# Performance work log

Measured on AMD Instinct MI355X. Metric: run time of the kernel, lower is better.

## Reference

```python
import jax, jax.numpy as jnp
import numpy as np

NH, NOPE_D, ROPE_D, V_D, R = 16, 48, 16, 64, 128
EPS = 1e-6

def rms_norm(x, w):
    norm = jax.lax.rsqrt(jnp.mean(jnp.square(x), axis=-1, keepdims=True) + EPS)
    return x * norm * w

def apply_rope(x, cos, sin):
    # x: (..., rope_d); cos/sin broadcastable (..., rope_d//2)
    d = x.shape[-1]
    x1, x2 = x[..., : d // 2], x[..., d // 2 :]
    return jnp.concatenate([x1 * cos - x2 * sin, x2 * cos + x1 * sin], axis=-1)

def setup_inputs() -> dict:
    key = jax.random.key(0)
    ks = jax.random.split(key, 8)
    B, T, D = 2, 2048, 1024
    s = lambda fan_in: 1.0 / np.sqrt(fan_in)
    return {
        "x": jax.random.normal(ks[0], (B, T, D), jnp.float32),
        "cos": jax.random.uniform(ks[1], (T, ROPE_D // 2), jnp.float32),
        "sin": jax.random.uniform(ks[2], (T, ROPE_D // 2), jnp.float32),
        "Wq": jax.random.normal(ks[3], (NH * (NOPE_D + ROPE_D), D), jnp.float32) * s(D),
        "q_norm_w": jnp.ones((NOPE_D + ROPE_D,), jnp.float32),
        "Wkva": jax.random.normal(ks[4], (R + ROPE_D, D), jnp.float32) * s(D),
        "kva_norm_w": jnp.ones((R,), jnp.float32),
        "Wkvb": jax.random.normal(ks[5], (NH * (NOPE_D + V_D), R), jnp.float32) * s(R),
        "Wo": jax.random.normal(ks[6], (D, NH * V_D), jnp.float32) * s(NH * V_D),
    }

def reference(x, cos, sin, Wq, q_norm_w, Wkva, kva_norm_w, Wkvb, Wo):
    B, T, D = x.shape
    # Q path: project, per-head RMSNorm over (nope+rope) dims, split
    q = (x @ Wq.T).reshape(B, T, NH, NOPE_D + ROPE_D)
    q = rms_norm(q, q_norm_w)
    q_nope, q_rope = q[..., :NOPE_D], q[..., NOPE_D:]
    # Low-rank KV path
    kv_a = x @ Wkva.T  # (B,T,R+ROPE_D)
    kv_latent = rms_norm(kv_a[..., :R], kva_norm_w)
    k_rope_raw = kv_a[..., R:]  # (B,T,ROPE_D) shared across heads
    kv_b = (kv_latent @ Wkvb.T).reshape(B, T, NH, NOPE_D + V_D)
    k_nope, v = kv_b[..., :NOPE_D], kv_b[..., NOPE_D:]
    # Decoupled RoPE
    cos_t = cos[None, :T, None, :]  # (1,T,1,rope_d/2)
    sin_t = sin[None, :T, None, :]
    q_rope = apply_rope(q_rope, cos_t, sin_t)
    k_rope = apply_rope(k_rope_raw[:, :, None, :], cos[None, :T, None, :], sin[None, :T, None, :])
    k_rope = jnp.broadcast_to(k_rope, (B, T, NH, ROPE_D))
    q_full = jnp.concatenate([q_nope, q_rope], axis=-1)  # (B,T,NH,64)
    k_full = jnp.concatenate([k_nope, k_rope], axis=-1)
    # Causal attention, scale = 1/sqrt(nope+rope)
    scale = (NOPE_D + ROPE_D) ** -0.5
    scores = jnp.einsum("bqhd,bkhd->bhqk", q_full, k_full) * scale
    causal = jnp.tril(jnp.ones((T, T), bool))
    scores = jnp.where(causal[None, None], scores, -jnp.inf)
    attn = jax.nn.softmax(scores, axis=-1)
    out = jnp.einsum("bhqk,bkhd->bqhd", attn, v).reshape(B, T, NH * V_D)
    return out @ Wo.T
```

## Files before the change

kernel.cpp:

```cpp
#include <hip/hip_runtime.h>
#include <hip/hip_bf16.h>
#include <math.h>

#define NH 16
#define T_ 2048
#define B_ 2
#define D_ 1024
#define EPS 1e-6f

typedef __attribute__((ext_vector_type(8))) short bf16x8;
typedef __attribute__((ext_vector_type(4))) float f32x4;

__device__ __forceinline__ float wred_sum(float v){
  #pragma unroll
  for (int o = 32; o > 0; o >>= 1) v += __shfl_xor(v, o, 64);
  return v;
}

__device__ __forceinline__ unsigned pack_bf16(float a, float b){
  __hip_bfloat162 t = __float22bfloat162_rn(make_float2(a, b));
  unsigned r; __builtin_memcpy(&r, &t, 4); return r;
}

__device__ __forceinline__ void gload_lds16(const void* g, void* l){
  __builtin_amdgcn_global_load_lds((const __attribute__((address_space(1))) void*)g,
                                   (__attribute__((address_space(3))) void*)l, 16, 0, 0);
}

__global__ __launch_bounds__(256)
void cvt5(const float* __restrict__ x, const float* __restrict__ wq,
          const float* __restrict__ wkva, const float* __restrict__ wkvb,
          const float* __restrict__ wo,
          __hip_bfloat16* __restrict__ xb, __hip_bfloat16* __restrict__ wqb,
          __hip_bfloat16* __restrict__ wkvab, __hip_bfloat16* __restrict__ wkvbb,
          __hip_bfloat16* __restrict__ wob)
{
  const int i = blockIdx.x * 256 + threadIdx.x;
  const float* s; __hip_bfloat16* d; size_t soff, doff;
  if      (i < 1048576) { s = x;    d = xb;    soff = doff = i; }
  else if (i < 1310720) { s = wq;   d = wqb;   soff = doff = i - 1048576; }
  else if (i < 1347584) { s = wkva; d = wkvab; soff = doff = i - 1310720; }
  else if (i < 1404928) {
    const int off = i - 1347584;
    const int srow = off >> 5, c4 = off & 31;
    const int h = srow / 112, dd = srow % 112;
    const int drow = (dd < 48) ? (h*48 + dd) : (768 + h*64 + (dd - 48));
    s = wkvb; d = wkvbb; soff = off; doff = (size_t)drow*32 + c4;
  }
  else                  { s = wo;   d = wob;   soff = doff = i - 1404928; }
  float4 v = *(const float4*)(s + soff * 4);
  *(__hip_bfloat162*)(d + doff * 4)     = __float22bfloat162_rn(make_float2(v.x, v.y));
  *(__hip_bfloat162*)(d + doff * 4 + 2) = __float22bfloat162_rn(make_float2(v.z, v.w));
}

template<typename CT>
__global__ __launch_bounds__(256, 2)
void gemm_bt64(const __hip_bfloat16* __restrict__ A, const __hip_bfloat16* __restrict__ W,
               CT* __restrict__ C, int M, int N, int K)
{
  __shared__ __hip_bfloat16 As[2][128 * 64];
  __shared__ __hip_bfloat16 Ws[2][64 * 64];
  const int tid = threadIdx.x;
  const int wv = tid >> 6, lane = tid & 63;
  const int m = lane & 15, quad = lane >> 4;
  const int bm = blockIdx.y * 128, bn = blockIdx.x * 64;

  const __hip_bfloat16* ga[4];
  const __hip_bfloat16* gw[2];
  #pragma unroll
  for (int i = 0; i < 4; i++) {
    const int slot = i*256 + tid;
    const int row = slot >> 3, cb = slot & 7;
    ga[i] = A + (size_t)(bm + row) * K + ((cb ^ (row & 7)) << 3);
  }
  #pragma unroll
  for (int i = 0; i < 2; i++) {
    const int slot = i*256 + tid;
    const int row = slot >> 3, cb = slot & 7;
    int wr = bn + row; if (wr >= N) wr = N - 1;
    gw[i] = W + (size_t)wr * K + ((cb ^ (row & 7)) << 3);
  }
  auto stage = [&](int buf){
    #pragma unroll
    for (int i = 0; i < 4; i++) { gload_lds16(ga[i], &As[buf][(i*256 + wv*64)*8]); ga[i] += 64; }
    #pragma unroll
    for (int i = 0; i < 2; i++) { gload_lds16(gw[i], &Ws[buf][(i*256 + wv*64)*8]); gw[i] += 64; }
  };

  f32x4 acc[2][4];
  #pragma unroll
  for (int mi = 0; mi < 2; mi++)
    #pragma unroll
    for (int nj = 0; nj < 4; nj++) acc[mi][nj] = (f32x4){0.f,0.f,0.f,0.f};

  stage(0);
  const int iters = K >> 6;
  for (int it = 0; it < iters; it++) {
    const int cur = it & 1;
    __syncthreads();
    if (it + 1 < iters) stage(cur ^ 1);
    #pragma unroll
    for (int ks = 0; ks < 2; ks++) {
      const int cb = ((ks*4 + quad) ^ (m & 7)) << 3;
      bf16x8 af[2], wf[4];
      #pragma unroll
      for (int mi = 0; mi < 2; mi++)
        af[mi] = *(const bf16x8*)(&As[cur][(wv*32 + mi*16 + m) * 64 + cb]);
      #pragma unroll
      for (int nj = 0; nj < 4; nj++)
        wf[nj] = *(const bf16x8*)(&Ws[cur][(nj*16 + m) * 64 + cb]);
      #pragma unroll
      for (int mi = 0; mi < 2; mi++)
        #pragma unroll
        for (int nj = 0; nj < 4; nj++)
          acc[mi][nj] = __builtin_amdgcn_mfma_f32_16x16x32_bf16(af[mi], wf[nj], acc[mi][nj], 0, 0, 0);
    }
  }

  #pragma unroll
  for (int mi = 0; mi < 2; mi++)
    #pragma unroll
    for (int nj = 0; nj < 4; nj++) {
      const int col = bn + nj*16 + m;
      if (col < N) {
        #pragma unroll
        for (int r = 0; r < 4; r++) {
          const int row = bm + wv*32 + mi*16 + quad*4 + r;
          if constexpr (sizeof(CT) == 2)
            C[(size_t)row * N + col] = (CT)__float2bfloat16(acc[mi][nj][r]);
          else
            C[(size_t)row * N + col] = acc[mi][nj][r];
        }
      }
    }
}

__global__ __launch_bounds__(256, 2)
void gemm_qkva(const __hip_bfloat16* __restrict__ A, const __hip_bfloat16* __restrict__ Wqb,
               const __hip_bfloat16* __restrict__ Wkvab,
               const float* __restrict__ qw, const float* __restrict__ cosp,
               const float* __restrict__ sinp,
               __hip_bfloat16* __restrict__ qb, float* __restrict__ kva)
{
  __shared__ __hip_bfloat16 As[2][128 * 64];
  __shared__ __hip_bfloat16 Ws[2][64 * 64];
  const int K = 1024;
  const int tid = threadIdx.x;
  const int wv = tid >> 6, lane = tid & 63;
  const int m = lane & 15, quad = lane >> 4;
  const int bm = blockIdx.y * 128;
  const bool isq = blockIdx.x < 16;
  const __hip_bfloat16* W = isq ? Wqb : Wkvab;
  const int bn = isq ? blockIdx.x*64 : (blockIdx.x - 16)*64;
  const int Nw = isq ? 1024 : 144;

  const __hip_bfloat16* ga[4];
  const __hip_bfloat16* gw[2];
  #pragma unroll
  for (int i = 0; i < 4; i++) {
    const int slot = i*256 + tid;
    const int row = slot >> 3, cb = slot & 7;
    ga[i] = A + (size_t)(bm + row) * K + ((cb ^ (row & 7)) << 3);
  }
  #pragma unroll
  for (int i = 0; i < 2; i++) {
    const int slot = i*256 + tid;
    const int row = slot >> 3, cb = slot & 7;
    int wr = bn + row; if (wr >= Nw) wr = Nw - 1;
    gw[i] = W + (size_t)wr * K + ((cb ^ (row & 7)) << 3);
  }
  auto stage = [&](int buf){
    #pragma unroll
    for (int i = 0; i < 4; i++) { gload_lds16(ga[i], &As[buf][(i*256 + wv*64)*8]); ga[i] += 64; }
    #pragma unroll
    for (int i = 0; i < 2; i++) { gload_lds16(gw[i], &Ws[buf][(i*256 + wv*64)*8]); gw[i] += 64; }
  };

  f32x4 acc[2][4];
  #pragma unroll
  for (int mi = 0; mi < 2; mi++)
    #pragma unroll
    for (int nj = 0; nj < 4; nj++) acc[mi][nj] = (f32x4){0.f,0.f,0.f,0.f};

  stage(0);
  for (int it = 0; it < 16; it++) {
    const int cur = it & 1;
    __syncthreads();
    if (it < 15) stage(cur ^ 1);
    #pragma unroll
    for (int ks = 0; ks < 2; ks++) {
      const int cb = ((ks*4 + quad) ^ (m & 7)) << 3;
      bf16x8 af[2], wf[4];
      #pragma unroll
      for (int mi = 0; mi < 2; mi++)
        af[mi] = *(const bf16x8*)(&As[cur][(wv*32 + mi*16 + m) * 64 + cb]);
      #pragma unroll
      for (int nj = 0; nj < 4; nj++)
        wf[nj] = *(const bf16x8*)(&Ws[cur][(nj*16 + m) * 64 + cb]);
      #pragma unroll
      for (int mi = 0; mi < 2; mi++)
        #pragma unroll
        for (int nj = 0; nj < 4; nj++)
          acc[mi][nj] = __builtin_amdgcn_mfma_f32_16x16x32_bf16(af[mi], wf[nj], acc[mi][nj], 0, 0, 0);
    }
  }

  if (isq) {
    const int head = blockIdx.x;
    float qwv[4];
    #pragma unroll
    for (int nj = 0; nj < 4; nj++) qwv[nj] = qw[nj*16 + m];
    const int j = m & 7;
    #pragma unroll
    for (int mi = 0; mi < 2; mi++) {
      #pragma unroll
      for (int r = 0; r < 4; r++) {
        float ss = 0.f;
        #pragma unroll
        for (int nj = 0; nj < 4; nj++) { const float t = acc[mi][nj][r]; ss = fmaf(t, t, ss); }
        ss += __shfl_xor(ss, 1, 64); ss += __shfl_xor(ss, 2, 64);
        ss += __shfl_xor(ss, 4, 64); ss += __shfl_xor(ss, 8, 64);
        const float nrm = rsqrtf(ss * (1.0f/64.0f) + EPS);
        float v[4];
        #pragma unroll
        for (int nj = 0; nj < 4; nj++) v[nj] = acc[mi][nj][r] * nrm * qwv[nj];
        const int grow = bm + wv*32 + mi*16 + quad*4 + r;
        const int t = grow & (T_ - 1);
        const int b = grow >> 11;
        const float part = __shfl_xor(v[3], 8, 64);
        const float c = cosp[t*8 + j], sn = sinp[t*8 + j];
        v[3] = (m < 8) ? (v[3]*c - part*sn) : (v[3]*c + part*sn);
        __hip_bfloat16* dst = qb + ((size_t)(b*NH + head)*T_ + t)*64 + m;
        #pragma unroll
        for (int nj = 0; nj < 4; nj++) dst[nj*16] = __float2bfloat16(v[nj] * 0.125f);
      }
    }
  } else {
    #pragma unroll
    for (int mi = 0; mi < 2; mi++)
      #pragma unroll
      for (int nj = 0; nj < 4; nj++) {
        const int col = bn + nj*16 + m;
        if (col < 144) {
          #pragma unroll
          for (int r = 0; r < 4; r++) {
            const int row = bm + wv*32 + mi*16 + quad*4 + r;
            kva[(size_t)row * 144 + col] = acc[mi][nj][r];
          }
        }
      }
  }
}

__global__ void prep_kv(const float* __restrict__ kva, const float* __restrict__ kw,
                        const float* __restrict__ cosp, const float* __restrict__ sinp,
                        __hip_bfloat16* __restrict__ kvl16, __hip_bfloat16* __restrict__ krope16)
{
  const int tid = threadIdx.x;
  const int bt = blockIdx.x;
  const int t = bt % T_;
  const float* row = kva + (size_t)bt * 144;
  const float v = row[tid];
  float s = wred_sum(v * v);
  __shared__ float red[2];
  if ((tid & 63) == 0) red[tid >> 6] = s;
  __syncthreads();
  const float total = red[0] + red[1];
  const float norm = rsqrtf(total * (1.0f/128.0f) + EPS);
  kvl16[(size_t)bt * 128 + tid] = __float2bfloat16(v * norm * kw[tid]);
  if (tid < 16) {
    const int j = tid & 7;
    const float c = cosp[t*8 + j], sn = sinp[t*8 + j];
    const float x1 = row[128 + j], x2 = row[136 + j];
    krope16[(size_t)bt * 16 + tid] = __float2bfloat16((tid < 8) ? (x1 * c - x2 * sn)
                                                               : (x2 * c + x1 * sn));
  }
}

__global__ __launch_bounds__(256, 2)
void gemm_kvb(const __hip_bfloat16* __restrict__ A, const __hip_bfloat16* __restrict__ W,
              __hip_bfloat16* __restrict__ knope, __hip_bfloat16* __restrict__ vt)
{
  __shared__ __hip_bfloat16 As[2][128 * 64];
  __shared__ __hip_bfloat16 Ws[2][64 * 64];
  const int K = 128;
  const int tid = threadIdx.x;
  const int wv = tid >> 6, lane = tid & 63;
  const int m = lane & 15, quad = lane >> 4;
  const int bm = blockIdx.y * 128, bn = blockIdx.x * 64;

  const __hip_bfloat16* ga[4];
  const __hip_bfloat16* gw[2];
  #pragma unroll
  for (int i = 0; i < 4; i++) {
    const int slot = i*256 + tid;
    const int row = slot >> 3, cb = slot & 7;
    ga[i] = A + (size_t)(bm + row) * K + ((cb ^ (row & 7)) << 3);
  }
  #pragma unroll
  for (int i = 0; i < 2; i++) {
    const int slot = i*256 + tid;
    const int row = slot >> 3, cb = slot & 7;
    gw[i] = W + (size_t)(bn + row) * K + ((cb ^ (row & 7)) << 3);
  }
  auto stage = [&](int buf){
    #pragma unroll
    for (int i = 0; i < 4; i++) { gload_lds16(ga[i], &As[buf][(i*256 + wv*64)*8]); ga[i] += 64; }
    #pragma unroll
    for (int i = 0; i < 2; i++) { gload_lds16(gw[i], &Ws[buf][(i*256 + wv*64)*8]); gw[i] += 64; }
  };

  f32x4 acc[2][4];
  #pragma unroll
  for (int mi = 0; mi < 2; mi++)
    #pragma unroll
    for (int nj = 0; nj < 4; nj++) acc[mi][nj] = (f32x4){0.f,0.f,0.f,0.f};

  stage(0);
  for (int it = 0; it < 2; it++) {
    const int cur = it & 1;
    __syncthreads();
    if (it == 0) stage(1);
    #pragma unroll
    for (int ks = 0; ks < 2; ks++) {
      const int cb = ((ks*4 + quad) ^ (m & 7)) << 3;
      bf16x8 af[2], wf[4];
      #pragma unroll
      for (int mi = 0; mi < 2; mi++)
        af[mi] = *(const bf16x8*)(&As[cur][(wv*32 + mi*16 + m) * 64 + cb]);
      #pragma unroll
      for (int nj = 0; nj < 4; nj++)
        wf[nj] = *(const bf16x8*)(&Ws[cur][(nj*16 + m) * 64 + cb]);
      #pragma unroll
      for (int mi = 0; mi < 2; mi++)
        #pragma unroll
        for (int nj = 0; nj < 4; nj++)
          acc[mi][nj] = __builtin_amdgcn_mfma_f32_16x16x32_bf16(af[mi], wf[nj], acc[mi][nj], 0, 0, 0);
    }
  }

  if (bn < 768) {
    #pragma unroll
    for (int mi = 0; mi < 2; mi++)
      #pragma unroll
      for (int nj = 0; nj < 4; nj++) {
        const int col = bn + nj*16 + m;
        #pragma unroll
        for (int r = 0; r < 4; r++) {
          const int row = bm + wv*32 + mi*16 + quad*4 + r;
          knope[(size_t)row * 768 + col] = __float2bfloat16(acc[mi][nj][r]);
        }
      }
  } else {
    __syncthreads();
    short* TL = (short*)&As[0][0];
    #pragma unroll
    for (int mi = 0; mi < 2; mi++)
      #pragma unroll
      for (int nj = 0; nj < 4; nj++) {
        const int d = nj*16 + m;
        #pragma unroll
        for (int r = 0; r < 4; r++) {
          const int tl = wv*32 + mi*16 + quad*4 + r;
          __hip_bfloat16 hv = __float2bfloat16(acc[mi][nj][r]);
          short sv; __builtin_memcpy(&sv, &hv, 2);
          TL[d*136 + tl] = sv;
        }
      }
    __syncthreads();
    const int h = (bn - 768) >> 6;
    const int b = bm >> 11;
    const int t0 = bm & (T_ - 1);
    #pragma unroll
    for (int i = 0; i < 4; i++) {
      const int unit = i*256 + tid;
      const int d = unit >> 4, tu = unit & 15;
      *(bf16x8*)(vt + ((size_t)(b*NH + h)*64 + d)*T_ + t0 + tu*8)
          = *(const bf16x8*)(TL + d*136 + tu*8);
    }
  }
}

__device__ __forceinline__ void fa_softmax(f32x4 (&s)[8], const bool diag,
    const int k0, const int qglob, const int m, const int quad,
    float& mrun, float& lrun, f32x4 (&o)[4], bf16x8 (&a)[4])
{
  if (diag) {
    #pragma unroll
    for (int sub = 0; sub < 8; sub++)
      #pragma unroll
      for (int r = 0; r < 4; r++)
        if (k0 + sub*16 + quad*4 + r > qglob) s[sub][r] = -1e30f;
  }
  float tm = -3.0e38f;
  #pragma unroll
  for (int sub = 0; sub < 8; sub++)
    #pragma unroll
    for (int r = 0; r < 4; r++) tm = fmaxf(tm, s[sub][r]);
  tm = fmaxf(tm, __shfl_xor(tm, 16, 64));
  tm = fmaxf(tm, __shfl_xor(tm, 32, 64));
  const float mn = fmaxf(mrun, tm);
  const float alpha = __expf(mrun - mn);
  float rs = 0.f;
  float p[8][4];
  #pragma unroll
  for (int sub = 0; sub < 8; sub++)
    #pragma unroll
    for (int r = 0; r < 4; r++) {
      const float e = __expf(s[sub][r] - mn);
      p[sub][r] = e; rs += e;
    }
  rs += __shfl_xor(rs, 16, 64);
  rs += __shfl_xor(rs, 32, 64);
  lrun = lrun * alpha + rs;
  mrun = mn;

  unsigned u[8][2];
  #pragma unroll
  for (int sub = 0; sub < 8; sub++) {
    u[sub][0] = pack_bf16(p[sub][0], p[sub][1]);
    u[sub][1] = pack_bf16(p[sub][2], p[sub][3]);
  }
  #pragma unroll
  for (int c = 0; c < 4; c++) {
    union { int i[4]; bf16x8 v; } au;
    #pragma unroll
    for (int w4 = 0; w4 < 4; w4++) {
      const int src = (((2*quad + (w4 >> 1)) & 3) << 4) | m;
      const int lo = __shfl((int)u[c*2][w4 & 1], src, 64);
      const int hi = __shfl((int)u[c*2+1][w4 & 1], src, 64);
      au.i[w4] = (quad & 2) ? hi : lo;
    }
    a[c] = au.v;
  }

  float al[4];
  #pragma unroll
  for (int r = 0; r < 4; r++) al[r] = __shfl(alpha, (quad << 2) | r, 64);
  #pragma unroll
  for (int vs = 0; vs < 4; vs++)
    #pragma unroll
    for (int r = 0; r < 4; r++) o[vs][r] *= al[r];
}

__device__ __forceinline__ void fa_store(float lrun, f32x4 (&oacc)[4],
    const int b, const int qrow0, const int h, const int m, const int quad,
    __hip_bfloat16* __restrict__ aout)
{
  float lr[4];
  #pragma unroll
  for (int r = 0; r < 4; r++) lr[r] = __shfl(lrun, (quad << 2) | r, 64);
  #pragma unroll
  for (int vs = 0; vs < 4; vs++)
    #pragma unroll
    for (int r = 0; r < 4; r++)
      aout[(size_t)(b*T_ + qrow0 + quad*4 + r) * 1024 + h*64 + vs*16 + m]
          = __float2bfloat16(oacc[vs][r] / lr[r]);
}

__global__ __launch_bounds__(256, 2)
void attn_pair2(const __hip_bfloat16* __restrict__ qb,
                const __hip_bfloat16* __restrict__ knope,
                const __hip_bfloat16* __restrict__ krope16,
                const __hip_bfloat16* __restrict__ vt16,
                __hip_bfloat16* __restrict__ aout)
{
  __shared__ __hip_bfloat16 SL[32768];
  const int tid = threadIdx.x;
  const int wv = tid >> 6, lane = tid & 63;
  const int m = lane & 15, quad = lane >> 4;
  const int ta = blockIdx.x;
  const int tb = 31 - ta;
  const int bh = blockIdx.y;
  const int b = bh >> 4, h = bh & 15;
  const int qbaseA = ta*64 + wv*16;
  const int qbaseB = tb*64 + wv*16;
  const int ntA = (ta + 2) >> 1;
  const int ntB = (tb + 2) >> 1;

  const __hip_bfloat16* qra = qb + ((size_t)bh*T_ + qbaseA + m)*64 + quad*8;
  const bf16x8 qA0 = *(const bf16x8*)qra, qA1 = *(const bf16x8*)(qra + 32);
  const __hip_bfloat16* qrb = qb + ((size_t)bh*T_ + qbaseB + m)*64 + quad*8;
  const bf16x8 qB0 = *(const bf16x8*)qrb, qB1 = *(const bf16x8*)(qrb + 32);

  const __hip_bfloat16* pK[4]; size_t iK[4];
  const __hip_bfloat16* pV[4];
  #pragma unroll
  for (int i = 0; i < 4; i++) {
    const int slot = i*256 + tid;
    const int krow = slot >> 3;
    const int kde = (slot & 7) ^ (krow & 7);
    if (kde < 6) { pK[i] = knope + (size_t)(b*T_ + krow)*768 + h*48 + kde*8; iK[i] = (size_t)128*768; }
    else         { pK[i] = krope16 + (size_t)(b*T_ + krow)*16 + (kde-6)*8;   iK[i] = (size_t)128*16; }
    const int vd = slot >> 4;
    const int vde = (slot & 15) ^ (vd & 7);
    pV[i] = vt16 + ((size_t)bh*64 + vd)*T_ + vde*8;
  }

  auto stage = [&](int buf){
    #pragma unroll
    for (int i = 0; i < 4; i++) {
      gload_lds16(pK[i], SL + buf*8192 + (i*256 + wv*64)*8);
      gload_lds16(pV[i], SL + 16384 + buf*8192 + (i*256 + wv*64)*8);
      pK[i] += iK[i]; pV[i] += 128;
    }
  };

  f32x4 oA[4], oB[4];
  #pragma unroll
  for (int vs = 0; vs < 4; vs++) { oA[vs] = (f32x4){0.f,0.f,0.f,0.f}; oB[vs] = (f32x4){0.f,0.f,0.f,0.f}; }
  float mA = -3.0e38f, lA = 0.f, mB = -3.0e38f, lB = 0.f;

  const int sw0 = quad ^ (m & 7);
  stage(0);

  for (int kt = 0; kt < ntB; kt++) {
    const int cur = kt & 1;
    __syncthreads();
    const __hip_bfloat16* Kc = SL + cur*8192;
    const __hip_bfloat16* Vc = SL + 16384 + cur*8192;
    const bool doA = (kt < ntA);

    f32x4 sA[8], sB[8];
    #pragma unroll
    for (int sub = 0; sub < 8; sub++) {
      const bf16x8 kf0 = *(const bf16x8*)(Kc + (sub*16 + m)*64 + sw0*8);
      const bf16x8 kf1 = *(const bf16x8*)(Kc + (sub*16 + m)*64 + (sw0^4)*8);
      f32x4 z = (f32x4){0.f,0.f,0.f,0.f};
      z = __builtin_amdgcn_mfma_f32_16x16x32_bf16(kf0, qB0, z, 0, 0, 0);
      z = __builtin_amdgcn_mfma_f32_16x16x32_bf16(kf1, qB1, z, 0, 0, 0);
      sB[sub] = z;
      if (doA) {
        f32x4 y = (f32x4){0.f,0.f,0.f,0.f};
        y = __builtin_amdgcn_mfma_f32_16x16x32_bf16(kf0, qA0, y, 0, 0, 0);
        y = __builtin_amdgcn_mfma_f32_16x16x32_bf16(kf1, qA1, y, 0, 0, 0);
        sA[sub] = y;
      }
    }

    if (kt + 1 < ntB) stage(cur ^ 1);

    bf16x8 aA[4], aB[4];
    fa_softmax(sB, kt == ntB-1, kt*128, qbaseB + m, m, quad, mB, lB, oB, aB);
    if (doA) fa_softmax(sA, kt == ntA-1, kt*128, qbaseA + m, m, quad, mA, lA, oA, aA);

    #pragma unroll
    for (int vs = 0; vs < 4; vs++) {
      #pragma unroll
      for (int c = 0; c < 4; c++) {
        const bf16x8 vf = *(const bf16x8*)(Vc + (vs*16 + m)*128 + (((c*4 + quad) ^ (m & 7)) << 3));
        oB[vs] = __builtin_amdgcn_mfma_f32_16x16x32_bf16(aB[c], vf, oB[vs], 0, 0, 0);
        if (doA) oA[vs] = __builtin_amdgcn_mfma_f32_16x16x32_bf16(aA[c], vf, oA[vs], 0, 0, 0);
      }
    }
  }

  fa_store(lA, oA, b, qbaseA, h, m, quad, aout);
  fa_store(lB, oB, b, qbaseB, h, m, quad, aout);
}

extern "C" void kernel_launch(void* const* d_in, const int* in_sizes, int n_in,
                              void* d_out, int out_size, void* d_ws, size_t ws_size,
                              hipStream_t stream)
{
  const float* x    = (const float*)d_in[0];
  const float* cosp = (const float*)d_in[1];
  const float* sinp = (const float*)d_in[2];
  const float* Wq   = (const float*)d_in[3];
  const float* qw   = (const float*)d_in[4];
  const float* Wkva = (const float*)d_in[5];
  const float* kw   = (const float*)d_in[6];
  const float* Wkvb = (const float*)d_in[7];
  const float* Wo   = (const float*)d_in[8];
  float* out = (float*)d_out;

  float* kva = (float*)d_ws;
  __hip_bfloat16* xb16    = (__hip_bfloat16*)(kva + 589824);
  __hip_bfloat16* knope16 = xb16 + 4194304;
  __hip_bfloat16* kvl16   = knope16 + 3145728;
  __hip_bfloat16* qb16    = kvl16 + 524288;
  __hip_bfloat16* vt16    = qb16 + 4194304;
  __hip_bfloat16* krope16 = vt16 + 4194304;
  __hip_bfloat16* Wqb     = krope16 + 65536;
  __hip_bfloat16* Wkvab   = Wqb + 1048576;
  __hip_bfloat16* Wkvbb   = Wkvab + 147456;
  __hip_bfloat16* Wob     = Wkvbb + 229376;
  __hip_bfloat16* ab16    = Wob + 1048576;

  const int M = B_ * T_;

  cvt5<<<6512, 256, 0, stream>>>(x, Wq, Wkva, Wkvb, Wo, xb16, Wqb, Wkvab, Wkvbb, Wob);
  gemm_qkva<<<dim3(19, 32), 256, 0, stream>>>(xb16, Wqb, Wkvab, qw, cosp, sinp, qb16, kva);
  prep_kv<<<M, 128, 0, stream>>>(kva, kw, cosp, sinp, kvl16, krope16);
  gemm_kvb<<<dim3(28, 32), 256, 0, stream>>>(kvl16, Wkvbb, knope16, vt16);
  attn_pair2<<<dim3(16, B_ * NH), 256, 0, stream>>>(qb16, knope16, krope16, vt16, ab16);
  gemm_bt64<float><<<dim3(16, 32), 256, 0, stream>>>(ab16, Wob, out, M, 1024, 1024);
}
```

Before: 190.8 us.

## Replace paired-tile attention with single-tile kernel at higher occupancy

```diff
diff --git a/kernel.cpp b/kernel.cpp
--- a/kernel.cpp
+++ b/kernel.cpp
@@ -381,68 +381,6 @@
   }
 }
 
-__device__ __forceinline__ void fa_softmax(f32x4 (&s)[8], const bool diag,
-    const int k0, const int qglob, const int m, const int quad,
-    float& mrun, float& lrun, f32x4 (&o)[4], bf16x8 (&a)[4])
-{
-  if (diag) {
-    #pragma unroll
-    for (int sub = 0; sub < 8; sub++)
-      #pragma unroll
-      for (int r = 0; r < 4; r++)
-        if (k0 + sub*16 + quad*4 + r > qglob) s[sub][r] = -1e30f;
-  }
-  float tm = -3.0e38f;
-  #pragma unroll
-  for (int sub = 0; sub < 8; sub++)
-    #pragma unroll
-    for (int r = 0; r < 4; r++) tm = fmaxf(tm, s[sub][r]);
-  tm = fmaxf(tm, __shfl_xor(tm, 16, 64));
-  tm = fmaxf(tm, __shfl_xor(tm, 32, 64));
-  const float mn = fmaxf(mrun, tm);
-  const float alpha = __expf(mrun - mn);
-  float rs = 0.f;
-  float p[8][4];
-  #pragma unroll
-  for (int sub = 0; sub < 8; sub++)
-    #pragma unroll
-    for (int r = 0; r < 4; r++) {
-      const float e = __expf(s[sub][r] - mn);
-      p[sub][r] = e; rs += e;
-    }
-  rs += __shfl_xor(rs, 16, 64);
-  rs += __shfl_xor(rs, 32, 64);
-  lrun = lrun * alpha + rs;
-  mrun = mn;
-
-  unsigned u[8][2];
-  #pragma unroll
-  for (int sub = 0; sub < 8; sub++) {
-    u[sub][0] = pack_bf16(p[sub][0], p[sub][1]);
-    u[sub][1] = pack_bf16(p[sub][2], p[sub][3]);
-  }
-  #pragma unroll
-  for (int c = 0; c < 4; c++) {
-    union { int i[4]; bf16x8 v; } au;
-    #pragma unroll
-    for (int w4 = 0; w4 < 4; w4++) {
-      const int src = (((2*quad + (w4 >> 1)) & 3) << 4) | m;
-      const int lo = __shfl((int)u[c*2][w4 & 1], src, 64);
-      const int hi = __shfl((int)u[c*2+1][w4 & 1], src, 64);
-      au.i[w4] = (quad & 2) ? hi : lo;
-    }
-    a[c] = au.v;
-  }
-
-  float al[4];
-  #pragma unroll
-  for (int r = 0; r < 4; r++) al[r] = __shfl(alpha, (quad << 2) | r, 64);
-  #pragma unroll
-  for (int vs = 0; vs < 4; vs++)
-    #pragma unroll
-    for (int r = 0; r < 4; r++) o[vs][r] *= al[r];
-}
-
 __device__ __forceinline__ void fa_store(float lrun, f32x4 (&oacc)[4],
     const int b, const int qrow0, const int h, const int m, const int quad,
     __hip_bfloat16* __restrict__ aout)
@@ -458,30 +396,25 @@
           = __float2bfloat16(oacc[vs][r] / lr[r]);
 }
 
-__global__ __launch_bounds__(256, 2)
-void attn_pair2(const __hip_bfloat16* __restrict__ qb,
-                const __hip_bfloat16* __restrict__ knope,
-                const __hip_bfloat16* __restrict__ krope16,
-                const __hip_bfloat16* __restrict__ vt16,
-                __hip_bfloat16* __restrict__ aout)
-{
-  __shared__ __hip_bfloat16 SL[32768];
+__global__ __launch_bounds__(256, 4)
+void attn_single(const __hip_bfloat16* __restrict__ qb,
+                 const __hip_bfloat16* __restrict__ knope,
+                 const __hip_bfloat16* __restrict__ krope16,
+                 const __hip_bfloat16* __restrict__ vt16,
+                 __hip_bfloat16* __restrict__ aout)
+{
+  __shared__ __hip_bfloat16 SL[16384];
   const int tid = threadIdx.x;
   const int wv = tid >> 6, lane = tid & 63;
   const int m = lane & 15, quad = lane >> 4;
-  const int ta = blockIdx.x;
-  const int tb = 31 - ta;
+  const int tile = blockIdx.x;
   const int bh = blockIdx.y;
   const int b = bh >> 4, h = bh & 15;
-  const int qbaseA = ta*64 + wv*16;
-  const int qbaseB = tb*64 + wv*16;
-  const int ntA = (ta + 2) >> 1;
-  const int ntB = (tb + 2) >> 1;
-
-  const __hip_bfloat16* qra = qb + ((size_t)bh*T_ + qbaseA + m)*64 + quad*8;
-  const bf16x8 qA0 = *(const bf16x8*)qra, qA1 = *(const bf16x8*)(qra + 32);
-  const __hip_bfloat16* qrb = qb + ((size_t)bh*T_ + qbaseB + m)*64 + quad*8;
-  const bf16x8 qB0 = *(const bf16x8*)qrb, qB1 = *(const bf16x8*)(qrb + 32);
+  const int qbase = tile*64 + wv*16;
+  const int nt = (tile + 2) >> 1;
+
+  const __hip_bfloat16* qr = qb + ((size_t)bh*T_ + qbase + m)*64 + quad*8;
+  const bf16x8 q0 = *(const bf16x8*)qr, q1 = *(const bf16x8*)(qr + 32);
 
   const __hip_bfloat16* pK[4]; size_t iK[4];
   const __hip_bfloat16* pV[4];
@@ -497,66 +430,102 @@
     pV[i] = vt16 + ((size_t)bh*64 + vd)*T_ + vde*8;
   }
 
-  auto stage = [&](int buf){
+  f32x4 o[4];
+  #pragma unroll
+  for (int vs = 0; vs < 4; vs++) o[vs] = (f32x4){0.f,0.f,0.f,0.f};
+  float mrun = -3.0e38f, lrun = 0.f;
+  const int sw0 = quad ^ (m & 7);
+  const int qglob = qbase + m;
+
+  for (int kt = 0; kt < nt; kt++) {
     #pragma unroll
     for (int i = 0; i < 4; i++) {
-      gload_lds16(pK[i], SL + buf*8192 + (i*256 + wv*64)*8);
-      gload_lds16(pV[i], SL + 16384 + buf*8192 + (i*256 + wv*64)*8);
+      gload_lds16(pK[i], SL + (i*256 + wv*64)*8);
+      gload_lds16(pV[i], SL + 8192 + (i*256 + wv*64)*8);
       pK[i] += iK[i]; pV[i] += 128;
     }
-  };
-
-  f32x4 oA[4], oB[4];
-  #pragma unroll
-  for (int vs = 0; vs < 4; vs++) { oA[vs] = (f32x4){0.f,0.f,0.f,0.f}; oB[vs] = (f32x4){0.f,0.f,0.f,0.f}; }
-  float mA = -3.0e38f, lA = 0.f, mB = -3.0e38f, lB = 0.f;
-
-  const int sw0 = quad ^ (m & 7);
-  stage(0);
-
-  for (int kt = 0; kt < ntB; kt++) {
-    const int cur = kt & 1;
     __syncthreads();
-    const __hip_bfloat16* Kc = SL + cur*8192;
-    const __hip_bfloat16* Vc = SL + 16384 + cur*8192;
-    const bool doA = (kt < ntA);
-
-    f32x4 sA[8], sB[8];
+
+    f32x4 s[8];
     #pragma unroll
     for (int sub = 0; sub < 8; sub++) {
-      const bf16x8 kf0 = *(const bf16x8*)(Kc + (sub*16 + m)*64 + sw0*8);
-      const bf16x8 kf1 = *(const bf16x8*)(Kc + (sub*16 + m)*64 + (sw0^4)*8);
+      const bf16x8 kf0 = *(const bf16x8*)(SL + (sub*16 + m)*64 + sw0*8);
+      const bf16x8 kf1 = *(const bf16x8*)(SL + (sub*16 + m)*64 + (sw0^4)*8);
       f32x4 z = (f32x4){0.f,0.f,0.f,0.f};
-      z = __builtin_amdgcn_mfma_f32_16x16x32_bf16(kf0, qB0, z, 0, 0, 0);
-      z = __builtin_amdgcn_mfma_f32_16x16x32_bf16(kf1, qB1, z, 0, 0, 0);
-      sB[sub] = z;
-      if (doA) {
-        f32x4 y = (f32x4){0.f,0.f,0.f,0.f};
-        y = __builtin_amdgcn_mfma_f32_16x16x32_bf16(kf0, qA0, y, 0, 0, 0);
-        y = __builtin_amdgcn_mfma_f32_16x16x32_bf16(kf1, qA1, y, 0, 0, 0);
-        sA[sub] = y;
-      }
-    }
-
-    if (kt + 1 < ntB) stage(cur ^ 1);
-
-    bf16x8 aA[4], aB[4];
-    fa_softmax(sB, kt == ntB-1, kt*128, qbaseB + m, m, quad, mB, lB, oB, aB);
-    if (doA) fa_softmax(sA, kt == ntA-1, kt*128, qbaseA + m, m, quad, mA, lA, oA, aA);
+      z = __builtin_amdgcn_mfma_f32_16x16x32_bf16(kf0, q0, z, 0, 0, 0);
+      z = __builtin_amdgcn_mfma_f32_16x16x32_bf16(kf1, q1, z, 0, 0, 0);
+      s[sub] = z;
+    }
+
+    if (kt == nt - 1) {
+      #pragma unroll
+      for (int sub = 0; sub < 8; sub++)
+        #pragma unroll
+        for (int r = 0; r < 4; r++)
+          if (kt*128 + sub*16 + quad*4 + r > qglob) s[sub][r] = -1e30f;
+    }
+    float tm = -3.0e38f;
+    #pragma unroll
+    for (int sub = 0; sub < 8; sub++)
+      #pragma unroll
+      for (int r = 0; r < 4; r++) tm = fmaxf(tm, s[sub][r]);
+    tm = fmaxf(tm, __shfl_xor(tm, 16, 64));
+    tm = fmaxf(tm, __shfl_xor(tm, 32, 64));
+    const float mn = fmaxf(mrun, tm);
+    const float alpha = __expf(mrun - mn);
+    float rs = 0.f;
+    #pragma unroll
+    for (int sub = 0; sub < 8; sub++)
+      #pragma unroll
+      for (int r = 0; r < 4; r++) {
+        const float e = __expf(s[sub][r] - mn);
+        s[sub][r] = e; rs += e;
+      }
+    rs += __shfl_xor(rs, 16, 64);
+    rs += __shfl_xor(rs, 32, 64);
+    lrun = lrun * alpha + rs;
+    mrun = mn;
+
+    unsigned u[8][2];
+    #pragma unroll
+    for (int sub = 0; sub < 8; sub++) {
+      u[sub][0] = pack_bf16(s[sub][0], s[sub][1]);
+      u[sub][1] = pack_bf16(s[sub][2], s[sub][3]);
+    }
+    bf16x8 a[4];
+    #pragma unroll
+    for (int c = 0; c < 4; c++) {
+      union { int i[4]; bf16x8 v; } au;
+      #pragma unroll
+      for (int w4 = 0; w4 < 4; w4++) {
+        const int src = (((2*quad + (w4 >> 1)) & 3) << 4) | m;
+        const int lo = __shfl((int)u[c*2][w4 & 1], src, 64);
+        const int hi = __shfl((int)u[c*2+1][w4 & 1], src, 64);
+        au.i[w4] = (quad & 2) ? hi : lo;
+      }
+      a[c] = au.v;
+    }
+
+    float al[4];
+    #pragma unroll
+    for (int r = 0; r < 4; r++) al[r] = __shfl(alpha, (quad << 2) | r, 64);
+    #pragma unroll
+    for (int vs = 0; vs < 4; vs++)
+      #pragma unroll
+      for (int r = 0; r < 4; r++) o[vs][r] *= al[r];
 
     #pragma unroll
     for (int vs = 0; vs < 4; vs++) {
       #pragma unroll
       for (int c = 0; c < 4; c++) {
-        const bf16x8 vf = *(const bf16x8*)(Vc + (vs*16 + m)*128 + (((c*4 + quad) ^ (m & 7)) << 3));
-        oB[vs] = __builtin_amdgcn_mfma_f32_16x16x32_bf16(aB[c], vf, oB[vs], 0, 0, 0);
-        if (doA) oA[vs] = __builtin_amdgcn_mfma_f32_16x16x32_bf16(aA[c], vf, oA[vs], 0, 0, 0);
-      }
-    }
-  }
-
-  fa_store(lA, oA, b, qbaseA, h, m, quad, aout);
-  fa_store(lB, oB, b, qbaseB, h, m, quad, aout);
+        const bf16x8 vf = *(const bf16x8*)(SL + 8192 + (vs*16 + m)*128 + (((c*4 + quad) ^ (m & 7)) << 3));
+        o[vs] = __builtin_amdgcn_mfma_f32_16x16x32_bf16(a[c], vf, o[vs], 0, 0, 0);
+      }
+    }
+    if (kt + 1 < nt) __syncthreads();
+  }
+
+  fa_store(lrun, o, b, qbase, h, m, quad, aout);
 }
 
 extern "C" void kernel_launch(void* const* d_in, const int* in_sizes, int n_in,
@@ -593,6 +562,6 @@
   gemm_qkva<<<dim3(19, 32), 256, 0, stream>>>(xb16, Wqb, Wkvab, qw, cosp, sinp, qb16, kva);
   prep_kv<<<M, 128, 0, stream>>>(kva, kw, cosp, sinp, kvl16, krope16);
   gemm_kvb<<<dim3(28, 32), 256, 0, stream>>>(kvl16, Wkvbb, knope16, vt16);
-  attn_pair2<<<dim3(16, B_ * NH), 256, 0, stream>>>(qb16, knope16, krope16, vt16, ab16);
+  attn_single<<<dim3(32, B_ * NH), 256, 0, stream>>>(qb16, knope16, krope16, vt16, ab16);
   gemm_bt64<float><<<dim3(16, 32), 256, 0, stream>>>(ab16, Wob, out, M, 1024, 1024);
 }
```

New measurement: 213.9 us. 1.12x slower.
